# Performance work log

Measured on AMD Instinct MI355X. Metric: run time of the kernel, lower is better.

## Reference

```python
import jax, jax.numpy as jnp
import numpy as np

IN_FEATURES = 4096
OUT_FEATURES = 11008
INTERLEAVE = 4
KSTRIDE = 64

# Inverse of the per-32-column AWQ shuffle applied in pack_int4_weight.
# Forward shuffle (on a length-32 index vector):
#   step1: reshape(4,4,2).transpose(1,0,2)  (swap axes 2,3 of [N,Kg,4,4,2])
#   step2: reshape(4,4,2).transpose(0,2,1)  (swap last two axes)
_a = np.arange(32)
_s1 = _a.reshape(4, 4, 2).transpose(1, 0, 2).reshape(32)
_s2p = _a.reshape(4, 4, 2).transpose(0, 2, 1).reshape(32)
_PERM32 = _s1[_s2p]            # shuffled[i] = orig[_PERM32[i]]
INV32 = np.argsort(_PERM32)     # orig[j] = shuffled[INV32[j]]


def setup_inputs() -> dict:
    key = jax.random.key(0)
    k1, k2, k3, k4, k5 = jax.random.split(key, 5)
    x = jax.random.normal(k1, (64, IN_FEATURES), dtype=jnp.float32)
    # Packed int4 weights: [N//interleave, K]; random 16-bit words unpack to
    # random int4 quant codes in [0, 15].
    qweight = jax.random.randint(
        k2, (OUT_FEATURES // INTERLEAVE, IN_FEATURES), 0, 65536, dtype=jnp.int32)
    scale = jax.random.uniform(k3, (OUT_FEATURES, 1), dtype=jnp.float32) * 0.01 + 1e-4
    zero_point = jax.random.uniform(k4, (OUT_FEATURES, 1), dtype=jnp.float32) * 15.0
    bias = jax.random.normal(k5, (OUT_FEATURES,), dtype=jnp.float32)
    return {"x": x, "qweight": qweight, "scale": scale,
            "zero_point": zero_point, "bias": bias}


def _unpack_int4(qweight):
    """Inverse of pack_int4_weight: [N//4, K] packed words -> [N, K] int4 codes."""
    Nq, K = qweight.shape
    N = Nq * INTERLEAVE
    p = qweight.astype(jnp.int32)
    # split nibbles: last axis is the interleave dim of the pack
    nib = jnp.stack([(p >> (4 * i)) & 0xF for i in range(INTERLEAVE)], axis=-1)  # [Nq, K, 4]
    # invert: [Nq, Kg, kstride, interleave] -> [Nq, Kg, interleave, kstride]
    nib = nib.reshape(Nq, K // KSTRIDE, KSTRIDE, INTERLEAVE)
    nib = nib.reshape(Nq, K // KSTRIDE, INTERLEAVE, KSTRIDE)
    # invert transpose(0,2,1,3) that moved interleave inside
    nib = nib.transpose(0, 2, 1, 3).reshape(N, K)
    # invert the per-32-column shuffle
    q = nib.reshape(N, K // 32, 32)[..., jnp.asarray(INV32)].reshape(N, K)
    return q


def reference(x, qweight, scale, zero_point, bias):
    q = _unpack_int4(qweight)
    q = jnp.clip(q, 0, 15).astype(jnp.float32)          # asymmetric 4-bit codes
    w = (q - zero_point) * scale                         # [N, K] dequantized weight
    return x @ w.T + bias                                # F.linear(x, w, bias)
```

## Files before the change

### kernel.cpp

```cpp
#include <hip/hip_runtime.h>
#include <hip/hip_bf16.h>

#define K_DIM 4096
#define N_DIM 11008

typedef __attribute__((ext_vector_type(4))) float f32x4;
typedef _Float16 half8 __attribute__((ext_vector_type(8)));
typedef _Float16 half2v __attribute__((ext_vector_type(2)));
typedef unsigned int uint32;

__global__ __launch_bounds__(256) void prep_x(const float* __restrict__ x,
                                              unsigned short* __restrict__ xp) {
    const int g = blockIdx.x * 256 + threadIdx.x;
    const int lane = g & 63, mt = (g >> 6) & 3, h = (g >> 8) & 1, kg = g >> 9;
    const int m = mt * 16 + (lane & 15), qq = lane >> 4;
    union { unsigned short v[8]; uint4 u4; } r;
#pragma unroll
    for (int e = 0; e < 8; ++e) {
        const int kp = h * 32 + qq * 8 + e;
        const int t = kp >> 2, ip = kp & 3;
        const int i = ((ip & 1) << 1) | (ip >> 1);
        const int col = ((t >> 3) << 5) + (t & 7) + (i << 3);
        const _Float16 hf = (_Float16)x[m * K_DIM + kg * 64 + col];
        r.v[e] = __builtin_bit_cast(unsigned short, hf);
    }
    *(uint4*)(xp + (size_t)g * 8) = r.u4;
}

__device__ __forceinline__ half8 build_bfrag(int w0, int w1, half2v s2, half2v c2) {
    union { half8 h; half2v p[4]; } r;
    const half2v k1024 = {(_Float16)1024.0f, (_Float16)1024.0f};
    const uint32 u0 = (uint32)(w0 & 0xF)        | (((uint32)w0 & 0xF00u) << 8) | 0x64006400u;
    const uint32 u1 = (uint32)((w0 >> 4) & 0xF) | (((uint32)w0 & 0xF000u) << 4) | 0x64006400u;
    const uint32 u2 = (uint32)(w1 & 0xF)        | (((uint32)w1 & 0xF00u) << 8) | 0x64006400u;
    const uint32 u3 = (uint32)((w1 >> 4) & 0xF) | (((uint32)w1 & 0xF000u) << 4) | 0x64006400u;
    half2v q;
    q = __builtin_bit_cast(half2v, u0) - k1024; r.p[0] = q * s2 + c2;
    q = __builtin_bit_cast(half2v, u1) - k1024; r.p[1] = q * s2 + c2;
    q = __builtin_bit_cast(half2v, u2) - k1024; r.p[2] = q * s2 + c2;
    q = __builtin_bit_cast(half2v, u3) - k1024; r.p[3] = q * s2 + c2;
    return r.h;
}

__global__ __launch_bounds__(256) void w4_gemm(
    const unsigned short* __restrict__ xp,
    const int*   __restrict__ qw,
    const float* __restrict__ scale,
    const float* __restrict__ zp,
    f32x4*       __restrict__ ws)
{
    __shared__ f32x4 part[2048];

    const int tid = threadIdx.x, lane = tid & 63, j = tid >> 6;
    const int nl = lane & 15, q = lane >> 4;
    const int nx = blockIdx.x, ky = blockIdx.y;
    const int n0 = nx * 32;
    const int nnA = n0 + nl, nnB = n0 + 16 + nl;

    const float sA = scale[nnA], zA = zp[nnA];
    const float sB = scale[nnB], zB = zp[nnB];
    const _Float16 shA = (_Float16)sA, chA = (_Float16)(-zA * sA);
    const _Float16 shB = (_Float16)sB, chB = (_Float16)(-zB * sB);
    const half2v s2A = {shA, shA}, c2A = {chA, chA};
    const half2v s2B = {shB, shB}, c2B = {chB, chB};

    const int* qbA = qw + ((size_t)(nnA >> 2) * K_DIM) + ((nnA & 3) * 16) + 2 * q;
    const int* qbB = qw + ((size_t)(nnB >> 2) * K_DIM) + ((nnB & 3) * 16) + 2 * q;

    f32x4 acc[2][4] = {};

    const int kg0 = ky * 16 + j * 4;
#pragma unroll
    for (int it = 0; it < 4; ++it) {
        const int kg = kg0 + it;
        const int2 a0 = *(const int2*)(qbA + kg * 64);
        const int2 a1 = *(const int2*)(qbA + kg * 64 + 8);
        const int2 b0 = *(const int2*)(qbB + kg * 64);
        const int2 b1 = *(const int2*)(qbB + kg * 64 + 8);
        const unsigned short* ab = xp + (size_t)kg * 4096;

        const half8 bfA0 = build_bfrag(a0.x, a0.y, s2A, c2A);
        const half8 bfB0 = build_bfrag(b0.x, b0.y, s2B, c2B);
#pragma unroll
        for (int mt = 0; mt < 4; ++mt) {
            const half8 af = *(const half8*)(ab + mt * 512 + lane * 8);
            acc[0][mt] = __builtin_amdgcn_mfma_f32_16x16x32_f16(af, bfA0, acc[0][mt], 0, 0, 0);
            acc[1][mt] = __builtin_amdgcn_mfma_f32_16x16x32_f16(af, bfB0, acc[1][mt], 0, 0, 0);
        }
        const half8 bfA1 = build_bfrag(a1.x, a1.y, s2A, c2A);
        const half8 bfB1 = build_bfrag(b1.x, b1.y, s2B, c2B);
#pragma unroll
        for (int mt = 0; mt < 4; ++mt) {
            const half8 af = *(const half8*)(ab + (4 + mt) * 512 + lane * 8);
            acc[0][mt] = __builtin_amdgcn_mfma_f32_16x16x32_f16(af, bfA1, acc[0][mt], 0, 0, 0);
            acc[1][mt] = __builtin_amdgcn_mfma_f32_16x16x32_f16(af, bfB1, acc[1][mt], 0, 0, 0);
        }
    }

#pragma unroll
    for (int nt = 0; nt < 2; ++nt)
#pragma unroll
        for (int mt = 0; mt < 4; ++mt)
            part[((j * 2 + nt) * 4 + mt) * 64 + q * 16 + nl] = acc[nt][mt];
    __syncthreads();

    f32x4* wsb = ws + ((size_t)nx * 4 + ky) * 512;
#pragma unroll
    for (int ss = 0; ss < 2; ++ss) {
        const int s = tid + ss * 256;
        f32x4 v = part[s];
        v += part[512 + s];
        v += part[1024 + s];
        v += part[1536 + s];
        wsb[s] = v;
    }
}

__global__ __launch_bounds__(256) void reduce_k(
    const f32x4* __restrict__ ws,
    const float* __restrict__ bias,
    float*       __restrict__ out)
{
    const int nx = blockIdx.x, tid = threadIdx.x;
    const f32x4* wsb = ws + (size_t)nx * 4 * 512;
#pragma unroll
    for (int ss = 0; ss < 2; ++ss) {
        const int s = tid + ss * 256;
        f32x4 v = wsb[s];
        v += wsb[512 + s];
        v += wsb[1024 + s];
        v += wsb[1536 + s];
        const int nt = s >> 8, mt = (s >> 6) & 3, qq = (s >> 4) & 3, nl = s & 15;
        const int n = nx * 32 + nt * 16 + nl;
        const float bv = bias[n];
        const int m0 = mt * 16 + qq * 4;
#pragma unroll
        for (int r = 0; r < 4; ++r)
            out[(size_t)(m0 + r) * N_DIM + n] = v[r] + bv;
    }
}

extern "C" void kernel_launch(void* const* d_in, const int* in_sizes, int n_in,
                              void* d_out, int out_size, void* d_ws, size_t ws_size,
                              hipStream_t stream) {
    const float* x     = (const float*)d_in[0];
    const int*   qw    = (const int*)d_in[1];
    const float* scale = (const float*)d_in[2];
    const float* zp    = (const float*)d_in[3];
    const float* bias  = (const float*)d_in[4];
    float* out = (float*)d_out;

    unsigned short* xp = (unsigned short*)d_ws;
    f32x4* part_ws = (f32x4*)((char*)d_ws + (1 << 20));

    prep_x<<<128, 256, 0, stream>>>(x, xp);
    dim3 grid(344, 4);
    w4_gemm<<<grid, 256, 0, stream>>>(xp, qw, scale, zp, part_ws);
    reduce_k<<<344, 256, 0, stream>>>(part_ws, bias, out);
}
```

Before: 30.05 us.

## Widen GEMM tile to 64 columns and double-buffer packed weight loads

Each block now covers 64 output columns instead of 32. Every activation fragment loaded from xp feeds four MFMAs instead of two, and the grid is halved to 172x4 blocks. Packed weight words are prefetched one iteration ahead into a two-slot register buffer, and the shared-memory reduction runs in two passes to fit the larger accumulator set. The cost is higher register pressure (16 accumulators plus buffered loads) and fewer blocks, which may leave many of the MI355X's CUs idle.

```diff
diff --git a/kernel.cpp b/kernel.cpp
--- a/kernel.cpp
+++ b/kernel.cpp
@@ -54,65 +54,73 @@
     const int tid = threadIdx.x, lane = tid & 63, j = tid >> 6;
     const int nl = lane & 15, q = lane >> 4;
     const int nx = blockIdx.x, ky = blockIdx.y;
-    const int n0 = nx * 32;
-    const int nnA = n0 + nl, nnB = n0 + 16 + nl;
+    const int n0 = nx * 64;
 
-    const float sA = scale[nnA], zA = zp[nnA];
-    const float sB = scale[nnB], zB = zp[nnB];
-    const _Float16 shA = (_Float16)sA, chA = (_Float16)(-zA * sA);
-    const _Float16 shB = (_Float16)sB, chB = (_Float16)(-zB * sB);
-    const half2v s2A = {shA, shA}, c2A = {chA, chA};
-    const half2v s2B = {shB, shB}, c2B = {chB, chB};
+    half2v s2[4], c2[4];
+#pragma unroll
+    for (int s = 0; s < 4; ++s) {
+        const int nn = n0 + s * 16 + nl;
+        const float sc = scale[nn], z = zp[nn];
+        const _Float16 sh = (_Float16)sc, ch = (_Float16)(-z * sc);
+        s2[s] = half2v{sh, sh};
+        c2[s] = half2v{ch, ch};
+    }
 
-    const int* qbA = qw + ((size_t)(nnA >> 2) * K_DIM) + ((nnA & 3) * 16) + 2 * q;
-    const int* qbB = qw + ((size_t)(nnB >> 2) * K_DIM) + ((nnB & 3) * 16) + 2 * q;
+    const int* qb = qw + ((size_t)((n0 >> 2) + (nl >> 2)) * K_DIM) + ((nl & 3) * 16) + 2 * q;
 
-    f32x4 acc[2][4] = {};
+    f32x4 acc[4][4] = {};
+    const int kg0 = ky * 16 + j * 4;
 
-    const int kg0 = ky * 16 + j * 4;
+    int2 qa[2][2][4];
+    auto loadq = [&](int buf, int kg) {
+#pragma unroll
+        for (int s = 0; s < 4; ++s) {
+            qa[buf][0][s] = *(const int2*)(qb + (size_t)s * 4 * K_DIM + kg * 64);
+            qa[buf][1][s] = *(const int2*)(qb + (size_t)s * 4 * K_DIM + kg * 64 + 8);
+        }
+    };
+
+    loadq(0, kg0);
 #pragma unroll
     for (int it = 0; it < 4; ++it) {
-        const int kg = kg0 + it;
-        const int2 a0 = *(const int2*)(qbA + kg * 64);
-        const int2 a1 = *(const int2*)(qbA + kg * 64 + 8);
-        const int2 b0 = *(const int2*)(qbB + kg * 64);
-        const int2 b1 = *(const int2*)(qbB + kg * 64 + 8);
-        const unsigned short* ab = xp + (size_t)kg * 4096;
-
-        const half8 bfA0 = build_bfrag(a0.x, a0.y, s2A, c2A);
-        const half8 bfB0 = build_bfrag(b0.x, b0.y, s2B, c2B);
+        if (it < 3) loadq((it + 1) & 1, kg0 + it + 1);
+        const int b = it & 1;
+        const unsigned short* ab = xp + (size_t)(kg0 + it) * 4096;
 #pragma unroll
-        for (int mt = 0; mt < 4; ++mt) {
-            const half8 af = *(const half8*)(ab + mt * 512 + lane * 8);
-            acc[0][mt] = __builtin_amdgcn_mfma_f32_16x16x32_f16(af, bfA0, acc[0][mt], 0, 0, 0);
-            acc[1][mt] = __builtin_amdgcn_mfma_f32_16x16x32_f16(af, bfB0, acc[1][mt], 0, 0, 0);
-        }
-        const half8 bfA1 = build_bfrag(a1.x, a1.y, s2A, c2A);
-        const half8 bfB1 = build_bfrag(b1.x, b1.y, s2B, c2B);
+        for (int h = 0; h < 2; ++h) {
+            half8 bf[4];
 #pragma unroll
-        for (int mt = 0; mt < 4; ++mt) {
-            const half8 af = *(const half8*)(ab + (4 + mt) * 512 + lane * 8);
-            acc[0][mt] = __builtin_amdgcn_mfma_f32_16x16x32_f16(af, bfA1, acc[0][mt], 0, 0, 0);
-            acc[1][mt] = __builtin_amdgcn_mfma_f32_16x16x32_f16(af, bfB1, acc[1][mt], 0, 0, 0);
+            for (int s = 0; s < 4; ++s)
+                bf[s] = build_bfrag(qa[b][h][s].x, qa[b][h][s].y, s2[s], c2[s]);
+#pragma unroll
+            for (int mt = 0; mt < 4; ++mt) {
+                const half8 af = *(const half8*)(ab + (h * 4 + mt) * 512 + lane * 8);
+#pragma unroll
+                for (int s = 0; s < 4; ++s)
+                    acc[s][mt] = __builtin_amdgcn_mfma_f32_16x16x32_f16(af, bf[s], acc[s][mt], 0, 0, 0);
+            }
         }
     }
 
+    f32x4* wsb = ws + ((size_t)nx * 4 + ky) * 1024;
 #pragma unroll
-    for (int nt = 0; nt < 2; ++nt)
+    for (int p = 0; p < 2; ++p) {
 #pragma unroll
-        for (int mt = 0; mt < 4; ++mt)
-            part[((j * 2 + nt) * 4 + mt) * 64 + q * 16 + nl] = acc[nt][mt];
-    __syncthreads();
-
-    f32x4* wsb = ws + ((size_t)nx * 4 + ky) * 512;
+        for (int mtl = 0; mtl < 2; ++mtl)
 #pragma unroll
-    for (int ss = 0; ss < 2; ++ss) {
-        const int s = tid + ss * 256;
-        f32x4 v = part[s];
-        v += part[512 + s];
-        v += part[1024 + s];
-        v += part[1536 + s];
-        wsb[s] = v;
+            for (int s = 0; s < 4; ++s)
+                part[j * 512 + (mtl * 4 + s) * 64 + lane] = acc[s][p * 2 + mtl];
+        __syncthreads();
+#pragma unroll
+        for (int ss = 0; ss < 2; ++ss) {
+            const int slot = tid + ss * 256;
+            f32x4 v = part[slot];
+            v += part[512 + slot];
+            v += part[1024 + slot];
+            v += part[1536 + slot];
+            wsb[p * 512 + slot] = v;
+        }
+        if (p == 0) __syncthreads();
     }
 }
 
@@ -122,16 +130,19 @@
     float*       __restrict__ out)
 {
     const int nx = blockIdx.x, tid = threadIdx.x;
-    const f32x4* wsb = ws + (size_t)nx * 4 * 512;
+    const f32x4* wsb = ws + (size_t)nx * 4096;
 #pragma unroll
-    for (int ss = 0; ss < 2; ++ss) {
-        const int s = tid + ss * 256;
-        f32x4 v = wsb[s];
-        v += wsb[512 + s];
-        v += wsb[1024 + s];
-        v += wsb[1536 + s];
-        const int nt = s >> 8, mt = (s >> 6) & 3, qq = (s >> 4) & 3, nl = s & 15;
-        const int n = nx * 32 + nt * 16 + nl;
+    for (int uu = 0; uu < 4; ++uu) {
+        const int u = tid + uu * 256;
+        f32x4 v = wsb[u];
+        v += wsb[1024 + u];
+        v += wsb[2048 + u];
+        v += wsb[3072 + u];
+        const int p = u >> 9, slot = u & 511;
+        const int mtl = slot >> 8, s = (slot >> 6) & 3, lane = slot & 63;
+        const int qq = lane >> 4, nnl = lane & 15;
+        const int mt = p * 2 + mtl;
+        const int n = nx * 64 + s * 16 + nnl;
         const float bv = bias[n];
         const int m0 = mt * 16 + qq * 4;
 #pragma unroll
@@ -154,7 +165,7 @@
     f32x4* part_ws = (f32x4*)((char*)d_ws + (1 << 20));
 
     prep_x<<<128, 256, 0, stream>>>(x, xp);
-    dim3 grid(344, 4);
+    dim3 grid(172, 4);
     w4_gemm<<<grid, 256, 0, stream>>>(xp, qw, scale, zp, part_ws);
-    reduce_k<<<344, 256, 0, stream>>>(part_ws, bias, out);
+    reduce_k<<<172, 256, 0, stream>>>(part_ws, bias, out);
 }
```

Result: slower. 35.37 us (+17.7%).
